# Kernel optimization log

Hardware: AMD Instinct MI355X
Metric: run time of the kernel (lower is better)

## Reference

```python
import jax, jax.numpy as jnp
import numpy as np

L = 7          # window side (odd)
A = 0.3        # weight of average term
B = 0.7        # weight of differential term


def mex_hat(d):
    grid = (np.mgrid[:d, :d] - d // 2) * 1.0
    eucl = np.sqrt((grid ** 2).sum(0)) / d
    return (eucl * np.exp(-eucl)).astype(np.float32)  # (d, d)


def setup_inputs() -> dict:
    key = jax.random.key(0)
    x = jax.random.normal(key, (64, 1, 512, 512), dtype=jnp.float32)
    kernel = jnp.asarray(mex_hat(L).reshape(-1))  # (L*L,), matches unfold row-major order
    return {"x": x, "kernel": kernel}


def reference(x, kernel):
    # x: [B,1,n,n], kernel: [L*L]
    n = x.shape[2]
    pad = L // 2
    xp = jnp.pad(x, ((0, 0), (0, 0), (pad, pad), (pad, pad)))  # zero pad, as F.unfold
    mean_acc = jnp.zeros_like(x)
    diff_acc = jnp.zeros_like(x)
    # fixed 49-offset loop replaces the im2col buffer; each shift is a view-slice
    for i in range(L):
        for j in range(L):
            s = jax.lax.dynamic_slice(xp, (0, 0, i, j), x.shape)
            mean_acc = mean_acc + s
            diff_acc = diff_acc + kernel[i * L + j] * jax.nn.relu(s - x)
    average_term = jnp.exp(-mean_acc / (L * L))              # [B,1,n,n]
    differential_term = diff_acc                             # [B,1,n,n]
    mask = A * average_term + B * differential_term
    mask = mask / jnp.sqrt(jnp.sum(mask ** 2))               # global L2 norm
    out = jnp.where(x > mask, x, jnp.zeros_like(x))
    return out, average_term, differential_term
```

## Files before the change

kernel.cpp:

```cpp
#include <hip/hip_runtime.h>
#include <stdint.h>

#define IMG 512
constexpr int TX = 64, TY = 32, PADW = 3;
constexpr int SMW = TX + 2 * PADW;
constexpr int SMH = TY + 2 * PADW;
constexpr int SMS = SMW + 2;
constexpr float A_W = 0.3f, B_W = 0.7f;

#define W1  0.12383970f
#define W2  0.16507309f
#define W4  0.21470754f
#define W5  0.23209061f
#define W8  0.26975268f
#define W9  0.27918814f
#define W10 0.28754623f
#define W13 0.30773566f
#define W18 0.33061044f

__device__ constexpr float KW[7][7] = {
    { W18, W13, W10, W9,  W10, W13, W18 },
    { W13, W8,  W5,  W4,  W5,  W8,  W13 },
    { W10, W5,  W2,  W1,  W2,  W5,  W10 },
    { W9,  W4,  W1,  0.f, W1,  W4,  W9  },
    { W10, W5,  W2,  W1,  W2,  W5,  W10 },
    { W13, W8,  W5,  W4,  W5,  W8,  W13 },
    { W18, W13, W10, W9,  W10, W13, W18 },
};

constexpr float ksum_calc() {
    float s = 0.f;
    for (int i = 0; i < 7; ++i)
        for (int j = 0; j < 7; ++j) s += KW[i][j];
    return s;
}
constexpr float KSUM = ksum_calc();

__global__ __launch_bounds__(256) void li_pass1(
    const float* __restrict__ x,
    float* __restrict__ outMask,
    float* __restrict__ outAvg,
    float* __restrict__ outDiff,
    float* __restrict__ partials)
{
    __shared__ float sm[SMH * SMS];
    __shared__ float red[4];
    const int tid = threadIdx.x;

    const int bx = blockIdx.x, by = blockIdx.y, b = blockIdx.z;
    const size_t imgBase = (size_t)b * IMG * IMG;
    const int x0 = bx * TX, y0 = by * TY;

    for (int idx = tid; idx < SMH * SMW; idx += 256) {
        int ly = idx / SMW, lx = idx - ly * SMW;
        int gx = x0 - PADW + lx, gy = y0 - PADW + ly;
        float v = 0.f;
        if ((unsigned)gx < IMG && (unsigned)gy < IMG)
            v = x[imgBase + (size_t)gy * IMG + gx];
        sm[ly * SMS + lx] = v;
    }
    __syncthreads();

    const int tx  = tid & 63;
    const int r   = tid >> 6;
    const int ty0 = r * 8;

    float c[8], mean[8], T[8];
    #pragma unroll
    for (int k = 0; k < 8; ++k) {
        c[k] = sm[(ty0 + k + PADW) * SMS + tx + PADW];
        mean[k] = 0.f; T[k] = 0.f;
    }

    #pragma unroll
    for (int wy = 0; wy < 14; ++wy) {
        float s[7];
        const int base = (ty0 + wy) * SMS + tx;
        #pragma unroll
        for (int dx = 0; dx < 7; ++dx) s[dx] = sm[base + dx];
        float rowsum = ((s[0] + s[1]) + (s[2] + s[3])) + ((s[4] + s[5]) + s[6]);
        #pragma unroll
        for (int k = 0; k < 8; ++k) {
            const int dy = wy - k;
            if (dy >= 0 && dy < 7) {
                mean[k] += rowsum;
                #pragma unroll
                for (int dx = 0; dx < 7; ++dx) {
                    if (KW[dy][dx] != 0.f)
                        T[k] = fmaf(KW[dy][dx], fmaxf(s[dx], c[k]), T[k]);
                }
            }
        }
    }

    float local = 0.f;
    #pragma unroll
    for (int k = 0; k < 8; ++k) {
        float avg = __expf(mean[k] * (-1.f / 49.f));
        float d   = fmaf(-KSUM, c[k], T[k]);
        float m   = fmaf(A_W, avg, B_W * d);
        local = fmaf(m, m, local);
        size_t g = imgBase + (size_t)(y0 + ty0 + k) * IMG + (x0 + tx);
        outAvg[g]  = avg;
        outDiff[g] = d;
        outMask[g] = m;
    }

    float v = local;
    #pragma unroll
    for (int off = 32; off > 0; off >>= 1) v += __shfl_down(v, off);
    if ((tid & 63) == 0) red[tid >> 6] = v;
    __syncthreads();
    if (tid == 0) {
        size_t pb = ((size_t)b * gridDim.y + by) * gridDim.x + bx;
        partials[pb] = red[0] + red[1] + red[2] + red[3];
    }
}

__global__ __launch_bounds__(1024) void li_reduce(
    const float* __restrict__ partials, int n, float* __restrict__ total)
{
    __shared__ float red[16];
    int tid = threadIdx.x;
    float v = 0.f;
    for (int i = tid; i < n; i += 1024) v += partials[i];
    #pragma unroll
    for (int off = 32; off > 0; off >>= 1) v += __shfl_down(v, off);
    if ((tid & 63) == 0) red[tid >> 6] = v;
    __syncthreads();
    if (tid == 0) {
        float s = 0.f;
        #pragma unroll
        for (int i = 0; i < 16; ++i) s += red[i];
        *total = s;
    }
}

__global__ __launch_bounds__(256) void li_pass2(
    const float4* __restrict__ x, const float4* __restrict__ mask,
    float4* __restrict__ out, const float* __restrict__ total)
{
    const float inv = 1.0f / sqrtf(*total);
    int i = blockIdx.x * 256 + threadIdx.x;
    float4 xv = x[i];
    float4 mv = mask[i];
    float4 ov;
    ov.x = (xv.x > mv.x * inv) ? xv.x : 0.f;
    ov.y = (xv.y > mv.y * inv) ? xv.y : 0.f;
    ov.z = (xv.z > mv.z * inv) ? xv.z : 0.f;
    ov.w = (xv.w > mv.w * inv) ? xv.w : 0.f;
    out[i] = ov;
}

extern "C" void kernel_launch(void* const* d_in, const int* in_sizes, int n_in,
                              void* d_out, int out_size, void* d_ws, size_t ws_size,
                              hipStream_t stream)
{
    const float* x = (const float*)d_in[0];
    const int Nelem = in_sizes[0];
    const int batch = Nelem / (IMG * IMG);

    float* out     = (float*)d_out;
    float* outMask = out;
    float* outAvg  = out + (size_t)Nelem;
    float* outDiff = out + (size_t)2 * Nelem;

    float* partials = (float*)d_ws;
    const int nblocks = (IMG / TX) * (IMG / TY) * batch;
    float* total = partials + nblocks;

    dim3 g1(IMG / TX, IMG / TY, batch);
    li_pass1<<<g1, 256, 0, stream>>>(x, outMask, outAvg, outDiff, partials);
    li_reduce<<<1, 1024, 0, stream>>>(partials, nblocks, total);

    const int nvec = Nelem / 4;
    li_pass2<<<nvec / 256, 256, 0, stream>>>(
        (const float4*)x, (const float4*)outMask, (float4*)out, total);
}
```

Measured before the change: 307.4 us.

## Fuse stencil, reduction and mask into one persistent cooperative kernel

Replaces the three-kernel pipeline with a single cooperative persistent kernel. It computes the stencil tiles, reduces the squared-mask partials through a grid-wide sync, then applies the threshold by recomputing the mask from the stored avg and diff outputs. This removes two kernel launches and the separate write and reread of the mask buffer. In exchange it adds a grid sync, reduces parallelism to a power-of-two persistent grid, and rereads avg and diff, which may still be in L2. The original three-kernel path stays as a fallback.

```diff
diff --git a/kernel.cpp b/kernel.cpp
--- a/kernel.cpp
+++ b/kernel.cpp
@@ -1,11 +1,16 @@
 #include <hip/hip_runtime.h>
+#include <hip/hip_cooperative_groups.h>
 #include <stdint.h>
+
+namespace cg = cooperative_groups;
 
 #define IMG 512
 constexpr int TX = 64, TY = 32, PADW = 3;
 constexpr int SMW = TX + 2 * PADW;
 constexpr int SMH = TY + 2 * PADW;
 constexpr int SMS = SMW + 2;
+constexpr int NBX = IMG / TX;
+constexpr int NBY = IMG / TY;
 constexpr float A_W = 0.3f, B_W = 0.7f;
 
 #define W1  0.12383970f
@@ -36,35 +41,9 @@
 }
 constexpr float KSUM = ksum_calc();
 
-__global__ __launch_bounds__(256) void li_pass1(
-    const float* __restrict__ x,
-    float* __restrict__ outMask,
-    float* __restrict__ outAvg,
-    float* __restrict__ outDiff,
-    float* __restrict__ partials)
-{
-    __shared__ float sm[SMH * SMS];
-    __shared__ float red[4];
-    const int tid = threadIdx.x;
-
-    const int bx = blockIdx.x, by = blockIdx.y, b = blockIdx.z;
-    const size_t imgBase = (size_t)b * IMG * IMG;
-    const int x0 = bx * TX, y0 = by * TY;
-
-    for (int idx = tid; idx < SMH * SMW; idx += 256) {
-        int ly = idx / SMW, lx = idx - ly * SMW;
-        int gx = x0 - PADW + lx, gy = y0 - PADW + ly;
-        float v = 0.f;
-        if ((unsigned)gx < IMG && (unsigned)gy < IMG)
-            v = x[imgBase + (size_t)gy * IMG + gx];
-        sm[ly * SMS + lx] = v;
-    }
-    __syncthreads();
-
-    const int tx  = tid & 63;
-    const int r   = tid >> 6;
-    const int ty0 = r * 8;
-
+__device__ __forceinline__ void stencil8(const float* __restrict__ sm, int tx, int ty0,
+                                         float (&avgO)[8], float (&dO)[8])
+{
     float c[8], mean[8], T[8];
     #pragma unroll
     for (int k = 0; k < 8; ++k) {
@@ -93,16 +72,159 @@
         }
     }
 
+    #pragma unroll
+    for (int k = 0; k < 8; ++k) {
+        avgO[k] = __expf(mean[k] * (-1.f / 49.f));
+        dO[k]   = fmaf(-KSUM, c[k], T[k]);
+    }
+}
+
+__global__ __launch_bounds__(256, 4) void li_fused(
+    const float* __restrict__ x,
+    float* __restrict__ out,
+    float* __restrict__ outAvg,
+    float* __restrict__ outDiff,
+    float* __restrict__ partials,
+    int ntiles)
+{
+    __shared__ float sm[SMH * SMS];
+    __shared__ float red[4];
+    __shared__ float tot_sm;
+
+    const int tid = threadIdx.x;
+    const int bid = blockIdx.x;
+    const int nb  = gridDim.x;
+
+    const int tx  = tid & 63;
+    const int r   = tid >> 6;
+    const int ty0 = r * 8;
+
     float local = 0.f;
+
+    for (int t = bid; t < ntiles; t += nb) {
+        const int bx = t & (NBX - 1);
+        const int by = (t >> 3) & (NBY - 1);
+        const int b  = t >> 7;
+        const size_t imgBase = (size_t)b * IMG * IMG;
+        const int x0 = bx * TX, y0 = by * TY;
+
+        __syncthreads();
+        for (int idx = tid; idx < SMH * SMW; idx += 256) {
+            int ly = idx / SMW, lx = idx - ly * SMW;
+            int gx = x0 - PADW + lx, gy = y0 - PADW + ly;
+            float v = 0.f;
+            if ((unsigned)gx < IMG && (unsigned)gy < IMG)
+                v = x[imgBase + (size_t)gy * IMG + gx];
+            sm[ly * SMS + lx] = v;
+        }
+        __syncthreads();
+
+        float avgv[8], dv[8];
+        stencil8(sm, tx, ty0, avgv, dv);
+
+        #pragma unroll
+        for (int k = 0; k < 8; ++k) {
+            float m = fmaf(A_W, avgv[k], B_W * dv[k]);
+            local = fmaf(m, m, local);
+            size_t g = imgBase + (size_t)(y0 + ty0 + k) * IMG + (x0 + tx);
+            outAvg[g]  = avgv[k];
+            outDiff[g] = dv[k];
+        }
+    }
+
+    {
+        float v = local;
+        #pragma unroll
+        for (int off = 32; off > 0; off >>= 1) v += __shfl_down(v, off);
+        if ((tid & 63) == 0) red[tid >> 6] = v;
+        __syncthreads();
+        if (tid == 0) {
+            float s = red[0] + red[1] + red[2] + red[3];
+            __hip_atomic_store(&partials[bid], s, __ATOMIC_RELEASE,
+                               __HIP_MEMORY_SCOPE_AGENT);
+        }
+    }
+
+    cg::this_grid().sync();
+
+    {
+        float v = 0.f;
+        for (int i = tid; i < nb; i += 256)
+            v += __hip_atomic_load(&partials[i], __ATOMIC_ACQUIRE,
+                                   __HIP_MEMORY_SCOPE_AGENT);
+        #pragma unroll
+        for (int off = 32; off > 0; off >>= 1) v += __shfl_down(v, off);
+        if ((tid & 63) == 0) red[tid >> 6] = v;
+        __syncthreads();
+        if (tid == 0) tot_sm = red[0] + red[1] + red[2] + red[3];
+        __syncthreads();
+    }
+    const float inv = 1.0f / sqrtf(tot_sm);
+
+    for (int t = bid; t < ntiles; t += nb) {
+        const int bx = t & (NBX - 1);
+        const int by = (t >> 3) & (NBY - 1);
+        const int b  = t >> 7;
+        const size_t imgBase = (size_t)b * IMG * IMG;
+        const int x0 = bx * TX, y0 = by * TY;
+
+        for (int i = tid; i < (TX * TY) / 4; i += 256) {
+            int row = i >> 4;
+            int col = (i & 15) << 2;
+            size_t g = imgBase + (size_t)(y0 + row) * IMG + (x0 + col);
+            float4 xv = *reinterpret_cast<const float4*>(x + g);
+            float4 av = *reinterpret_cast<const float4*>(outAvg + g);
+            float4 dv = *reinterpret_cast<const float4*>(outDiff + g);
+            float4 ov;
+            ov.x = (xv.x > fmaf(A_W, av.x, B_W * dv.x) * inv) ? xv.x : 0.f;
+            ov.y = (xv.y > fmaf(A_W, av.y, B_W * dv.y) * inv) ? xv.y : 0.f;
+            ov.z = (xv.z > fmaf(A_W, av.z, B_W * dv.z) * inv) ? xv.z : 0.f;
+            ov.w = (xv.w > fmaf(A_W, av.w, B_W * dv.w) * inv) ? xv.w : 0.f;
+            *reinterpret_cast<float4*>(out + g) = ov;
+        }
+    }
+}
+
+__global__ __launch_bounds__(256) void li_pass1(
+    const float* __restrict__ x,
+    float* __restrict__ outMask,
+    float* __restrict__ outAvg,
+    float* __restrict__ outDiff,
+    float* __restrict__ partials)
+{
+    __shared__ float sm[SMH * SMS];
+    __shared__ float red[4];
+    const int tid = threadIdx.x;
+
+    const int bx = blockIdx.x, by = blockIdx.y, b = blockIdx.z;
+    const size_t imgBase = (size_t)b * IMG * IMG;
+    const int x0 = bx * TX, y0 = by * TY;
+
+    for (int idx = tid; idx < SMH * SMW; idx += 256) {
+        int ly = idx / SMW, lx = idx - ly * SMW;
+        int gx = x0 - PADW + lx, gy = y0 - PADW + ly;
+        float v = 0.f;
+        if ((unsigned)gx < IMG && (unsigned)gy < IMG)
+            v = x[imgBase + (size_t)gy * IMG + gx];
+        sm[ly * SMS + lx] = v;
+    }
+    __syncthreads();
+
+    const int tx  = tid & 63;
+    const int r   = tid >> 6;
+    const int ty0 = r * 8;
+
+    float avgv[8], dv[8];
+    stencil8(sm, tx, ty0, avgv, dv);
+
+    float local = 0.f;
     #pragma unroll
     for (int k = 0; k < 8; ++k) {
-        float avg = __expf(mean[k] * (-1.f / 49.f));
-        float d   = fmaf(-KSUM, c[k], T[k]);
-        float m   = fmaf(A_W, avg, B_W * d);
+        float m = fmaf(A_W, avgv[k], B_W * dv[k]);
         local = fmaf(m, m, local);
         size_t g = imgBase + (size_t)(y0 + ty0 + k) * IMG + (x0 + tx);
-        outAvg[g]  = avg;
-        outDiff[g] = d;
+        outAvg[g]  = avgv[k];
+        outDiff[g] = dv[k];
         outMask[g] = m;
     }
 
@@ -160,16 +282,47 @@
     const int Nelem = in_sizes[0];
     const int batch = Nelem / (IMG * IMG);
 
-    float* out     = (float*)d_out;
+    float* out      = (float*)d_out;
+    float* outAvg   = out + (size_t)Nelem;
+    float* outDiff  = out + (size_t)2 * Nelem;
+    float* partials = (float*)d_ws;
+
+    int ntiles = NBX * NBY * batch;
+
+    static int coop_nb = 0;
+    if (coop_nb == 0) {
+        int occ = 0, ncu = 0, dev = 0;
+        hipError_t e0 = hipGetDevice(&dev);
+        hipError_t e1 = hipOccupancyMaxActiveBlocksPerMultiprocessor(
+            &occ, reinterpret_cast<const void*>(&li_fused), 256, 0);
+        hipError_t e2 = hipDeviceGetAttribute(
+            &ncu, hipDeviceAttributeMultiprocessorCount, dev);
+        if (e0 == hipSuccess && e1 == hipSuccess && e2 == hipSuccess &&
+            occ > 0 && ncu > 0) {
+            int cap = occ * ncu;
+            int nb = 256;
+            while (nb * 2 <= cap && nb * 2 <= 2048) nb *= 2;
+            coop_nb = nb;
+        } else {
+            coop_nb = -1;
+        }
+    }
+
+    if (coop_nb > 0) {
+        void* kargs[] = { (void*)&x, (void*)&out, (void*)&outAvg,
+                          (void*)&outDiff, (void*)&partials, (void*)&ntiles };
+        hipError_t e = hipLaunchCooperativeKernel(
+            reinterpret_cast<const void*>(&li_fused),
+            dim3(coop_nb), dim3(256), kargs, 0, stream);
+        if (e == hipSuccess) return;
+        coop_nb = -1;
+    }
+
     float* outMask = out;
-    float* outAvg  = out + (size_t)Nelem;
-    float* outDiff = out + (size_t)2 * Nelem;
-
-    float* partials = (float*)d_ws;
-    const int nblocks = (IMG / TX) * (IMG / TY) * batch;
+    const int nblocks = NBX * NBY * batch;
     float* total = partials + nblocks;
 
-    dim3 g1(IMG / TX, IMG / TY, batch);
+    dim3 g1(NBX, NBY, batch);
     li_pass1<<<g1, 256, 0, stream>>>(x, outMask, outAvg, outDiff, partials);
     li_reduce<<<1, 1024, 0, stream>>>(partials, nblocks, total);
 
```

Result: slower. 500.9 us (+62.9%).

## Retile pass1 to 256x8 blocks with float4 loads, 2x4 per-thread outputs

Applied to the files above, without the earlier changes.

Each block now covers a wide 256x8 tile, and each thread computes a 2-row by 4-column patch instead of an 8-row column. Halo loads, shared-memory reads and output stores all use float4. Row sums are updated with a sliding window across the 4 columns. The aim is fewer global and LDS transactions and vectorized stores. In exchange, the vertical halo overhead grows (14 rows loaded for 8 output rows versus 38 for 32), there are more blocks, and there are more partials to reduce.

```diff
diff --git a/kernel.cpp b/kernel.cpp
--- a/kernel.cpp
+++ b/kernel.cpp
@@ -2,11 +2,13 @@
 #include <stdint.h>
 
 #define IMG 512
-constexpr int TX = 64, TY = 32, PADW = 3;
-constexpr int SMW = TX + 2 * PADW;
-constexpr int SMH = TY + 2 * PADW;
-constexpr int SMS = SMW + 2;
 constexpr float A_W = 0.3f, B_W = 0.7f;
+
+constexpr int TX = 256, TY = 8;
+constexpr int SMW = 264;
+constexpr int SMH = TY + 6;
+constexpr int NBX = IMG / TX;
+constexpr int NBY = IMG / TY;
 
 #define W1  0.12383970f
 #define W2  0.16507309f
@@ -43,7 +45,7 @@
     float* __restrict__ outDiff,
     float* __restrict__ partials)
 {
-    __shared__ float sm[SMH * SMS];
+    __shared__ float sm[SMH * SMW];
     __shared__ float red[4];
     const int tid = threadIdx.x;
 
@@ -51,43 +53,57 @@
     const size_t imgBase = (size_t)b * IMG * IMG;
     const int x0 = bx * TX, y0 = by * TY;
 
-    for (int idx = tid; idx < SMH * SMW; idx += 256) {
-        int ly = idx / SMW, lx = idx - ly * SMW;
-        int gx = x0 - PADW + lx, gy = y0 - PADW + ly;
-        float v = 0.f;
-        if ((unsigned)gx < IMG && (unsigned)gy < IMG)
-            v = x[imgBase + (size_t)gy * IMG + gx];
-        sm[ly * SMS + lx] = v;
+    for (int idx = tid; idx < SMH * (SMW / 4); idx += 256) {
+        const int ly = idx / (SMW / 4);
+        const int fx = idx - ly * (SMW / 4);
+        const int gy  = y0 - 3 + ly;
+        const int gxf = x0 - 4 + 4 * fx;
+        float4 v = make_float4(0.f, 0.f, 0.f, 0.f);
+        if ((unsigned)gy < IMG && (unsigned)gxf <= (IMG - 4))
+            v = *reinterpret_cast<const float4*>(&x[imgBase + (size_t)gy * IMG + gxf]);
+        *reinterpret_cast<float4*>(&sm[ly * SMW + 4 * fx]) = v;
     }
     __syncthreads();
 
-    const int tx  = tid & 63;
-    const int r   = tid >> 6;
-    const int ty0 = r * 8;
+    const int lane = tid & 63;
+    const int r2   = (tid >> 6) * 2;
+    const int c0   = lane * 4;
 
-    float c[8], mean[8], T[8];
-    #pragma unroll
-    for (int k = 0; k < 8; ++k) {
-        c[k] = sm[(ty0 + k + PADW) * SMS + tx + PADW];
-        mean[k] = 0.f; T[k] = 0.f;
-    }
+    float4 C0 = *reinterpret_cast<const float4*>(&sm[(r2 + 3) * SMW + c0 + 4]);
+    float4 C1 = *reinterpret_cast<const float4*>(&sm[(r2 + 4) * SMW + c0 + 4]);
+    const float C[2][4] = { { C0.x, C0.y, C0.z, C0.w },
+                            { C1.x, C1.y, C1.z, C1.w } };
+
+    float T[2][4]  = { {0.f,0.f,0.f,0.f}, {0.f,0.f,0.f,0.f} };
+    float MN[2][4] = { {0.f,0.f,0.f,0.f}, {0.f,0.f,0.f,0.f} };
 
     #pragma unroll
-    for (int wy = 0; wy < 14; ++wy) {
-        float s[7];
-        const int base = (ty0 + wy) * SMS + tx;
+    for (int j = 0; j < 8; ++j) {
+        const float4* smrow = reinterpret_cast<const float4*>(&sm[(r2 + j) * SMW + c0]);
+        const float4 a0 = smrow[0], a1 = smrow[1], a2 = smrow[2];
+        const float s[12] = { a0.x, a0.y, a0.z, a0.w,
+                              a1.x, a1.y, a1.z, a1.w,
+                              a2.x, a2.y, a2.z, a2.w };
+        float rs[4];
+        rs[0] = ((s[1] + s[2]) + (s[3] + s[4])) + ((s[5] + s[6]) + s[7]);
+        rs[1] = (rs[0] - s[1]) + s[8];
+        rs[2] = (rs[1] - s[2]) + s[9];
+        rs[3] = (rs[2] - s[3]) + s[10];
+
         #pragma unroll
-        for (int dx = 0; dx < 7; ++dx) s[dx] = sm[base + dx];
-        float rowsum = ((s[0] + s[1]) + (s[2] + s[3])) + ((s[4] + s[5]) + s[6]);
-        #pragma unroll
-        for (int k = 0; k < 8; ++k) {
-            const int dy = wy - k;
+        for (int k = 0; k < 2; ++k) {
+            const int dy = j - k;
             if (dy >= 0 && dy < 7) {
-                mean[k] += rowsum;
+                #pragma unroll
+                for (int c = 0; c < 4; ++c) MN[k][c] += rs[c];
                 #pragma unroll
                 for (int dx = 0; dx < 7; ++dx) {
-                    if (KW[dy][dx] != 0.f)
-                        T[k] = fmaf(KW[dy][dx], fmaxf(s[dx], c[k]), T[k]);
+                    if (KW[dy][dx] != 0.f) {
+                        #pragma unroll
+                        for (int c = 0; c < 4; ++c)
+                            T[k][c] = fmaf(KW[dy][dx],
+                                           fmaxf(s[c + dx + 1], C[k][c]), T[k][c]);
+                    }
                 }
             }
         }
@@ -95,15 +111,19 @@
 
     float local = 0.f;
     #pragma unroll
-    for (int k = 0; k < 8; ++k) {
-        float avg = __expf(mean[k] * (-1.f / 49.f));
-        float d   = fmaf(-KSUM, c[k], T[k]);
-        float m   = fmaf(A_W, avg, B_W * d);
-        local = fmaf(m, m, local);
-        size_t g = imgBase + (size_t)(y0 + ty0 + k) * IMG + (x0 + tx);
-        outAvg[g]  = avg;
-        outDiff[g] = d;
-        outMask[g] = m;
+    for (int k = 0; k < 2; ++k) {
+        float av[4], dv[4], mv[4];
+        #pragma unroll
+        for (int c = 0; c < 4; ++c) {
+            av[c] = __expf(MN[k][c] * (-1.f / 49.f));
+            dv[c] = fmaf(-KSUM, C[k][c], T[k][c]);
+            mv[c] = fmaf(A_W, av[c], B_W * dv[c]);
+            local = fmaf(mv[c], mv[c], local);
+        }
+        const size_t g = imgBase + (size_t)(y0 + r2 + k) * IMG + (x0 + c0);
+        *reinterpret_cast<float4*>(&outAvg[g])  = make_float4(av[0], av[1], av[2], av[3]);
+        *reinterpret_cast<float4*>(&outDiff[g]) = make_float4(dv[0], dv[1], dv[2], dv[3]);
+        *reinterpret_cast<float4*>(&outMask[g]) = make_float4(mv[0], mv[1], mv[2], mv[3]);
     }
 
     float v = local;
@@ -166,10 +186,10 @@
     float* outDiff = out + (size_t)2 * Nelem;
 
     float* partials = (float*)d_ws;
-    const int nblocks = (IMG / TX) * (IMG / TY) * batch;
+    const int nblocks = NBX * NBY * batch;
     float* total = partials + nblocks;
 
-    dim3 g1(IMG / TX, IMG / TY, batch);
+    dim3 g1(NBX, NBY, batch);
     li_pass1<<<g1, 256, 0, stream>>>(x, outMask, outAvg, outDiff, partials);
     li_reduce<<<1, 1024, 0, stream>>>(partials, nblocks, total);
 
```

After: 315.1 us. 2.5% more time.
